# Optimization experiments

Hardware: AMD Instinct MI355X
Metric: run time of the kernel (lower is better)

## Reference

```python
import math
import jax, jax.numpy as jnp
import numpy as np

H = 12  # n_heads
NEG = -1e9

def setup_inputs() -> dict:
    key = jax.random.key(0)
    ks = jax.random.split(key, 5)
    B, S, D = 1, 4096, 768
    x = jax.random.normal(ks[0], (B, S, D), dtype=jnp.float32)
    Wqkv = jax.random.normal(ks[1], (D, 3 * D), dtype=jnp.float32) * (1.0 / math.sqrt(D))
    bqkv = jnp.zeros((3 * D,), dtype=jnp.float32)
    Wout = jax.random.normal(ks[2], (D, D), dtype=jnp.float32) * (1.0 / math.sqrt(D))
    bout = jnp.zeros((D,), dtype=jnp.float32)
    rel_bias = jax.random.normal(ks[3], (H, S, S), dtype=jnp.float32) * 0.02
    # additive causal mask: 0 on/below diagonal, large negative above
    causal_mask = jnp.where(jnp.tril(jnp.ones((S, S), dtype=bool)), 0.0, NEG).astype(jnp.float32)
    return {"x": x, "Wqkv": Wqkv, "bqkv": bqkv, "Wout": Wout, "bout": bout,
            "rel_bias": rel_bias, "causal_mask": causal_mask}

def reference(x, Wqkv, bqkv, Wout, bout, rel_bias, causal_mask):
    B, S, D = x.shape
    hd = D // H
    qkv = x @ Wqkv + bqkv                      # [B,S,3D]
    q, k, v = jnp.split(qkv, 3, axis=-1)
    def heads(t):  # [B,S,D] -> [B,H,S,hd]
        return t.reshape(B, S, H, hd).transpose(0, 2, 1, 3)
    q, k, v = heads(q), heads(k), heads(v)
    scores = jnp.einsum('bhqd,bhkd->bhqk', q, k) / math.sqrt(hd)
    scores = scores + rel_bias[None] + causal_mask[None, None]
    attn = jax.nn.softmax(scores, axis=-1)     # dropout p=0.0 -> identity
    out = jnp.einsum('bhqk,bhkd->bhqd', attn, v)
    out = out.transpose(0, 2, 1, 3).reshape(B, S, D)
    return out @ Wout + bout
```

## Files before the change

### kernel.cpp

```cpp
#include <hip/hip_runtime.h>
#include <stdint.h>

typedef _Float16 f16;
typedef _Float16 f16x8 __attribute__((ext_vector_type(8)));
typedef _Float16 f16x4 __attribute__((ext_vector_type(4)));
typedef float f32x4 __attribute__((ext_vector_type(4)));

#define NEGF -1e30f

static __device__ __forceinline__ f32x4 mfma16(f16x8 a, f16x8 b, f32x4 c) {
    return __builtin_amdgcn_mfma_f32_16x16x32_f16(a, b, c, 0, 0, 0);
}

static __device__ __forceinline__ void gload_lds16(const void* g, void* l) {
    __builtin_amdgcn_global_load_lds(
        (const __attribute__((address_space(1))) unsigned int*)g,
        (__attribute__((address_space(3))) unsigned int*)l, 16, 0, 0);
}

__global__ void cast_f32_f16(const float* __restrict__ src, f16* __restrict__ dst, int n) {
    int idx = blockIdx.x * blockDim.x + threadIdx.x;
    int stride = gridDim.x * blockDim.x;
    for (int i = idx * 4; i < n; i += stride * 4) {
        float4 v = *(const float4*)(src + i);
        f16x4 h;
        h[0] = (f16)v.x; h[1] = (f16)v.y; h[2] = (f16)v.z; h[3] = (f16)v.w;
        *(f16x4*)(dst + i) = h;
    }
}

__global__ void transpose_cast(const float* __restrict__ src, f16* __restrict__ dst, int R, int C) {
    __shared__ float tile[32][33];
    const int c0 = blockIdx.x * 32, r0 = blockIdx.y * 32;
    const int tx = threadIdx.x & 31, ty = threadIdx.x >> 5;
#pragma unroll
    for (int i = 0; i < 32; i += 8)
        tile[ty + i][tx] = src[(size_t)(r0 + ty + i) * C + c0 + tx];
    __syncthreads();
#pragma unroll
    for (int i = 0; i < 32; i += 8)
        dst[(size_t)(c0 + ty + i) * R + r0 + tx] = (f16)tile[tx][ty + i];
}

template <int MODE>
__global__ void __launch_bounds__(256, 2)
gemm_f16(const f16* __restrict__ A, const f16* __restrict__ Bt,
         const float* __restrict__ bias,
         f16* __restrict__ Qb, f16* __restrict__ Kb, f16* __restrict__ Vtb,
         float* __restrict__ Cout, int K, int N) {
    __shared__ alignas(16) f16 As[128 * 32];
    __shared__ alignas(16) f16 Bs[128 * 32];
    const int t = threadIdx.x;
    const int lane = t & 63, wid = t >> 6;
    const int wm = wid >> 1, wn = wid & 1;
    const int lr = lane & 15, lg = lane >> 4;
    const int m0 = blockIdx.y * 128, n0 = blockIdx.x * 128;
    f32x4 acc[4][4] = {};
    for (int k0 = 0; k0 < K; k0 += 32) {
#pragma unroll
        for (int i = 0; i < 2; i++) {
            const int cc = t + i * 256;
            const int rr = cc >> 2, ch = cc & 3;
            gload_lds16(A + (size_t)(m0 + rr) * K + k0 + ch * 8, (f16*)As + cc * 8);
            gload_lds16(Bt + (size_t)(n0 + rr) * K + k0 + ch * 8, (f16*)Bs + cc * 8);
        }
        __syncthreads();
        f16x8 af[4], bf[4];
#pragma unroll
        for (int i = 0; i < 4; i++)
            af[i] = *(const f16x8*)(As + (wm * 64 + i * 16 + lr) * 32 + lg * 8);
#pragma unroll
        for (int j = 0; j < 4; j++)
            bf[j] = *(const f16x8*)(Bs + (wn * 64 + j * 16 + lr) * 32 + lg * 8);
#pragma unroll
        for (int i = 0; i < 4; i++)
#pragma unroll
            for (int j = 0; j < 4; j++)
                acc[i][j] = mfma16(af[i], bf[j], acc[i][j]);
        __syncthreads();
    }
#pragma unroll
    for (int i = 0; i < 4; i++) {
#pragma unroll
        for (int j = 0; j < 4; j++) {
            const int n_g = n0 + wn * 64 + j * 16 + lr;
            const float bv = bias[n_g];
#pragma unroll
            for (int jj = 0; jj < 4; jj++) {
                const int m_g = m0 + wm * 64 + i * 16 + lg * 4 + jj;
                const float val = acc[i][j][jj] + bv;
                if (MODE == 0) {
                    if (n_g < 768) {
                        Qb[(((n_g >> 6) * 4096) + m_g) * 64 + (n_g & 63)] = (f16)(val * 0.125f);
                    } else if (n_g < 1536) {
                        const int n2 = n_g - 768;
                        Kb[(((n2 >> 6) * 4096) + m_g) * 64 + (n2 & 63)] = (f16)val;
                    } else {
                        const int n2 = n_g - 1536;
                        Vtb[((n2 >> 6) * 64 + (n2 & 63)) * 4096 + m_g] = (f16)val;
                    }
                } else {
                    Cout[(size_t)m_g * N + n_g] = val;
                }
            }
        }
    }
}

__global__ void __launch_bounds__(256, 3)
attn_fwd(const f16* __restrict__ Qb, const f16* __restrict__ Kb,
         const f16* __restrict__ Vtb, const float* __restrict__ rel_bias,
         f16* __restrict__ Opart, float* __restrict__ mpart, float* __restrict__ lpart) {
    __shared__ alignas(16) f16 Ks[64 * 64];
    __shared__ alignas(16) f16 Vs[64 * 64];
    __shared__ alignas(16) f16 Ps[4][32 * 72];
    __shared__ alignas(16) float fac[4][32];
    const int bid = blockIdx.x;
    const int h = bid / 144;
    int rr = bid % 144;
    int qb = 0;
    for (;;) { const int n = (qb + 4) >> 2; if (rr < n) break; rr -= n; ++qb; }
    const int c = rr;
    const int lo = c * 8;
    const int hi = min(lo + 8, 2 * qb + 2);

    const int t = threadIdx.x, lane = t & 63, wid = t >> 6;
    const int lr = lane & 15, lg = lane >> 4;
    const int g = qb * 4 + wid;
    const int q0w = g * 32;
    const int ktd = g >> 1;
    const f16* Qh = Qb + (size_t)h * 4096 * 64;
    const f16* Kh = Kb + (size_t)h * 4096 * 64;
    const f16* Vh = Vtb + (size_t)h * 64 * 4096;
    const float* rbh = rel_bias + (size_t)h * 4096 * 4096;

    f16x8 qf[2][2];
#pragma unroll
    for (int nf = 0; nf < 2; nf++)
#pragma unroll
        for (int kd = 0; kd < 2; kd++)
            qf[nf][kd] = *(const f16x8*)(Qh + (size_t)(q0w + nf * 16 + lr) * 64 + kd * 32 + lg * 8);

    f32x4 o[2][4] = {};
    float mrow[2] = {NEGF, NEGF};
    float lrow[2] = {0.f, 0.f};

    for (int kt = lo; kt < hi; kt++) {
        const int kbase = kt * 64;
#pragma unroll
        for (int i = 0; i < 2; i++) {
            const int cc = t + i * 256;
            const int row = cc >> 3;
            const int cswz = (((cc & 7) * 16) ^ ((row & 7) << 4)) >> 1;
            gload_lds16(Kh + (size_t)(kbase + row) * 64 + cswz, (f16*)Ks + cc * 8);
            gload_lds16(Vh + (size_t)row * 4096 + kbase + cswz, (f16*)Vs + cc * 8);
        }
        __syncthreads();
        if (kt <= ktd) {
            float4 rb[2][4];
#pragma unroll
            for (int nf = 0; nf < 2; nf++)
#pragma unroll
                for (int mf = 0; mf < 4; mf++)
                    rb[nf][mf] = *(const float4*)(rbh + (size_t)(q0w + nf * 16 + lr) * 4096 + kbase + mf * 16 + lg * 4);
            f32x4 st[4][2] = {};
#pragma unroll
            for (int kd = 0; kd < 2; kd++) {
#pragma unroll
                for (int mf = 0; mf < 4; mf++) {
                    const int r = mf * 16 + lr;
                    const int cf = ((kd * 64 + lg * 16) ^ ((r & 7) << 4)) >> 1;
                    const f16x8 kf = *(const f16x8*)(Ks + r * 64 + cf);
#pragma unroll
                    for (int nf = 0; nf < 2; nf++)
                        st[mf][nf] = mfma16(kf, qf[nf][kd], st[mf][nf]);
                }
            }
            const bool diag = (kt == ktd);
#pragma unroll
            for (int nf = 0; nf < 2; nf++) {
                const int q_g = q0w + nf * 16 + lr;
                float mx = NEGF;
#pragma unroll
                for (int mf = 0; mf < 4; mf++) {
                    const float rbv[4] = {rb[nf][mf].x, rb[nf][mf].y, rb[nf][mf].z, rb[nf][mf].w};
#pragma unroll
                    for (int jj = 0; jj < 4; jj++) {
                        float v = st[mf][nf][jj] + rbv[jj];
                        if (diag) {
                            const int k_g = kbase + mf * 16 + lg * 4 + jj;
                            v = (k_g > q_g) ? NEGF : v;
                        }
                        st[mf][nf][jj] = v;
                        mx = fmaxf(mx, v);
                    }
                }
                mx = fmaxf(mx, __shfl_xor(mx, 16));
                mx = fmaxf(mx, __shfl_xor(mx, 32));
                const float mnew = fmaxf(mrow[nf], mx);
                const float fscale = __expf(mrow[nf] - mnew);
                mrow[nf] = mnew;
                float rsum = 0.f;
#pragma unroll
                for (int mf = 0; mf < 4; mf++) {
                    f16x4 pv;
#pragma unroll
                    for (int jj = 0; jj < 4; jj++) {
                        const float p = __expf(st[mf][nf][jj] - mnew);
                        rsum += p;
                        pv[jj] = (f16)p;
                    }
                    *(f16x4*)(&Ps[wid][(nf * 16 + lr) * 72 + mf * 16 + lg * 4]) = pv;
                }
                rsum += __shfl_xor(rsum, 16);
                rsum += __shfl_xor(rsum, 32);
                lrow[nf] = lrow[nf] * fscale + rsum;
                if (lane < 16) fac[wid][nf * 16 + lr] = fscale;
            }
            asm volatile("s_waitcnt lgkmcnt(0)" ::: "memory");
#pragma unroll
            for (int qf2 = 0; qf2 < 2; qf2++) {
                const float4 fv = *(const float4*)&fac[wid][qf2 * 16 + lg * 4];
                const float fvv[4] = {fv.x, fv.y, fv.z, fv.w};
#pragma unroll
                for (int df = 0; df < 4; df++)
#pragma unroll
                    for (int jj = 0; jj < 4; jj++)
                        o[qf2][df][jj] *= fvv[jj];
            }
#pragma unroll
            for (int kk = 0; kk < 2; kk++) {
                f16x8 pa[2], vb[4];
#pragma unroll
                for (int qf2 = 0; qf2 < 2; qf2++)
                    pa[qf2] = *(const f16x8*)(&Ps[wid][(qf2 * 16 + lr) * 72 + kk * 32 + lg * 8]);
#pragma unroll
                for (int df = 0; df < 4; df++) {
                    const int r = df * 16 + lr;
                    const int cf = ((kk * 64 + lg * 16) ^ ((r & 7) << 4)) >> 1;
                    vb[df] = *(const f16x8*)(Vs + r * 64 + cf);
                }
#pragma unroll
                for (int qf2 = 0; qf2 < 2; qf2++)
#pragma unroll
                    for (int df = 0; df < 4; df++)
                        o[qf2][df] = mfma16(pa[qf2], vb[df], o[qf2][df]);
            }
        }
        __syncthreads();
    }

    const int s = (h * 128 + g) * 8 + c;
    f16* Op = Opart + (size_t)s * 2048;
#pragma unroll
    for (int qf2 = 0; qf2 < 2; qf2++)
#pragma unroll
        for (int df = 0; df < 4; df++)
#pragma unroll
            for (int jj = 0; jj < 4; jj++)
                Op[(qf2 * 16 + lg * 4 + jj) * 64 + df * 16 + lr] = (f16)o[qf2][df][jj];
    if (lg == 0) {
#pragma unroll
        for (int nf = 0; nf < 2; nf++) {
            mpart[(size_t)s * 32 + nf * 16 + lr] = mrow[nf];
            lpart[(size_t)s * 32 + nf * 16 + lr] = lrow[nf];
        }
    }
}

__global__ void __launch_bounds__(256)
merge_norm(const f16* __restrict__ Opart, const float* __restrict__ mpart,
           const float* __restrict__ lpart, f16* __restrict__ Ob) {
    __shared__ float wls[8][32];
    __shared__ float Linv[32];
    const int g = blockIdx.x, h = blockIdx.y;
    const int nc = (g >> 4) + 1;
    const size_t sb = (size_t)(h * 128 + g) * 8;
    const int t = threadIdx.x;
    if (t < 32) {
        float M = NEGF;
#pragma unroll
        for (int i = 0; i < 8; i++)
            if (i < nc) M = fmaxf(M, mpart[(sb + i) * 32 + t]);
        float L = 0.f;
#pragma unroll
        for (int i = 0; i < 8; i++)
            if (i < nc) {
                const float w = __expf(mpart[(sb + i) * 32 + t] - M);
                wls[i][t] = w;
                L += w * lpart[(sb + i) * 32 + t];
            }
        Linv[t] = 1.f / L;
    }
    __syncthreads();
    const int row = t >> 3, dq = t & 7;
    float acc[8] = {};
#pragma unroll
    for (int i = 0; i < 8; i++) {
        if (i < nc) {
            const f16x8 a = *(const f16x8*)(Opart + (sb + i) * 2048 + row * 64 + dq * 8);
            const float w = wls[i][row];
#pragma unroll
            for (int j = 0; j < 8; j++) acc[j] += w * (float)a[j];
        }
    }
    const float inv = Linv[row];
    const int q = g * 32 + row;
    f16x8 ov;
#pragma unroll
    for (int j = 0; j < 8; j++) ov[j] = (f16)(acc[j] * inv);
    *(f16x8*)(Ob + (size_t)q * 768 + h * 64 + dq * 8) = ov;
}

extern "C" void kernel_launch(void* const* d_in, const int* in_sizes, int n_in,
                              void* d_out, int out_size, void* d_ws, size_t ws_size,
                              hipStream_t stream) {
    const float* x = (const float*)d_in[0];
    const float* Wqkv = (const float*)d_in[1];
    const float* bqkv = (const float*)d_in[2];
    const float* Wout = (const float*)d_in[3];
    const float* bout = (const float*)d_in[4];
    const float* rel_bias = (const float*)d_in[5];
    float* out = (float*)d_out;

    f16* p = (f16*)d_ws;
    f16* xb = p;     p += (size_t)4096 * 768;
    f16* WqkvT = p;  p += (size_t)2304 * 768;
    f16* WoutT = p;  p += (size_t)768 * 768;
    f16* Qb = p;     p += (size_t)12 * 4096 * 64;
    f16* Kb = p;     p += (size_t)12 * 4096 * 64;
    f16* Vtb = p;    p += (size_t)12 * 4096 * 64;
    f16* Ob = p;     p += (size_t)4096 * 768;
    f16* Opart = p;  p += (size_t)12 * 128 * 8 * 2048;
    float* fp = (float*)p;
    float* mpart = fp;  fp += (size_t)12 * 128 * 8 * 32;
    float* lpart = fp;  fp += (size_t)12 * 128 * 8 * 32;

    cast_f32_f16<<<3072, 256, 0, stream>>>(x, xb, 4096 * 768);
    transpose_cast<<<dim3(2304 / 32, 768 / 32), 256, 0, stream>>>(Wqkv, WqkvT, 768, 2304);
    transpose_cast<<<dim3(768 / 32, 768 / 32), 256, 0, stream>>>(Wout, WoutT, 768, 768);
    gemm_f16<0><<<dim3(18, 32), 256, 0, stream>>>(xb, WqkvT, bqkv, Qb, Kb, Vtb, nullptr, 768, 2304);
    attn_fwd<<<dim3(1728), 256, 0, stream>>>(Qb, Kb, Vtb, rel_bias, Opart, mpart, lpart);
    merge_norm<<<dim3(128, 12), 256, 0, stream>>>(Opart, mpart, lpart, Ob);
    gemm_f16<1><<<dim3(6, 32), 256, 0, stream>>>(Ob, WoutT, bout, nullptr, nullptr, nullptr, out, 768, 768);
}
```

Before: 225.1 us.

## Double-buffer LDS tiles in GEMMs and attention, retile output projection

```diff
diff --git a/kernel.cpp b/kernel.cpp
--- a/kernel.cpp
+++ b/kernel.cpp
@@ -42,36 +42,42 @@
         dst[(size_t)(c0 + ty + i) * R + r0 + tx] = (f16)tile[tx][ty + i];
 }
 
-template <int MODE>
 __global__ void __launch_bounds__(256, 2)
-gemm_f16(const f16* __restrict__ A, const f16* __restrict__ Bt,
+gemm_qkv(const f16* __restrict__ A, const f16* __restrict__ Bt,
          const float* __restrict__ bias,
-         f16* __restrict__ Qb, f16* __restrict__ Kb, f16* __restrict__ Vtb,
-         float* __restrict__ Cout, int K, int N) {
-    __shared__ alignas(16) f16 As[128 * 32];
-    __shared__ alignas(16) f16 Bs[128 * 32];
+         f16* __restrict__ Qb, f16* __restrict__ Kb, f16* __restrict__ Vtb, int K) {
+    __shared__ alignas(16) f16 As[2][128 * 32];
+    __shared__ alignas(16) f16 Bs[2][128 * 32];
     const int t = threadIdx.x;
     const int lane = t & 63, wid = t >> 6;
     const int wm = wid >> 1, wn = wid & 1;
     const int lr = lane & 15, lg = lane >> 4;
     const int m0 = blockIdx.y * 128, n0 = blockIdx.x * 128;
-    f32x4 acc[4][4] = {};
-    for (int k0 = 0; k0 < K; k0 += 32) {
+
+    auto stage = [&](int buf, int k0) {
 #pragma unroll
         for (int i = 0; i < 2; i++) {
             const int cc = t + i * 256;
             const int rr = cc >> 2, ch = cc & 3;
-            gload_lds16(A + (size_t)(m0 + rr) * K + k0 + ch * 8, (f16*)As + cc * 8);
-            gload_lds16(Bt + (size_t)(n0 + rr) * K + k0 + ch * 8, (f16*)Bs + cc * 8);
-        }
-        __syncthreads();
+            gload_lds16(A + (size_t)(m0 + rr) * K + k0 + ch * 8, (f16*)As[buf] + cc * 8);
+            gload_lds16(Bt + (size_t)(n0 + rr) * K + k0 + ch * 8, (f16*)Bs[buf] + cc * 8);
+        }
+    };
+
+    f32x4 acc[4][4] = {};
+    stage(0, 0);
+    __syncthreads();
+    const int NK = K / 32;
+    for (int it = 0; it < NK; ++it) {
+        const int cur = it & 1;
+        if (it + 1 < NK) stage(cur ^ 1, (it + 1) * 32);
         f16x8 af[4], bf[4];
 #pragma unroll
         for (int i = 0; i < 4; i++)
-            af[i] = *(const f16x8*)(As + (wm * 64 + i * 16 + lr) * 32 + lg * 8);
+            af[i] = *(const f16x8*)((f16*)As[cur] + (wm * 64 + i * 16 + lr) * 32 + lg * 8);
 #pragma unroll
         for (int j = 0; j < 4; j++)
-            bf[j] = *(const f16x8*)(Bs + (wn * 64 + j * 16 + lr) * 32 + lg * 8);
+            bf[j] = *(const f16x8*)((f16*)Bs[cur] + (wn * 64 + j * 16 + lr) * 32 + lg * 8);
 #pragma unroll
         for (int i = 0; i < 4; i++)
 #pragma unroll
@@ -89,19 +95,72 @@
             for (int jj = 0; jj < 4; jj++) {
                 const int m_g = m0 + wm * 64 + i * 16 + lg * 4 + jj;
                 const float val = acc[i][j][jj] + bv;
-                if (MODE == 0) {
-                    if (n_g < 768) {
-                        Qb[(((n_g >> 6) * 4096) + m_g) * 64 + (n_g & 63)] = (f16)(val * 0.125f);
-                    } else if (n_g < 1536) {
-                        const int n2 = n_g - 768;
-                        Kb[(((n2 >> 6) * 4096) + m_g) * 64 + (n2 & 63)] = (f16)val;
-                    } else {
-                        const int n2 = n_g - 1536;
-                        Vtb[((n2 >> 6) * 64 + (n2 & 63)) * 4096 + m_g] = (f16)val;
-                    }
+                if (n_g < 768) {
+                    Qb[(((n_g >> 6) * 4096) + m_g) * 64 + (n_g & 63)] = (f16)(val * 0.125f);
+                } else if (n_g < 1536) {
+                    const int n2 = n_g - 768;
+                    Kb[(((n2 >> 6) * 4096) + m_g) * 64 + (n2 & 63)] = (f16)val;
                 } else {
-                    Cout[(size_t)m_g * N + n_g] = val;
+                    const int n2 = n_g - 1536;
+                    Vtb[((n2 >> 6) * 64 + (n2 & 63)) * 4096 + m_g] = (f16)val;
                 }
+            }
+        }
+    }
+}
+
+__global__ void __launch_bounds__(256, 3)
+gemm_out(const f16* __restrict__ A, const f16* __restrict__ Bt,
+         const float* __restrict__ bias, float* __restrict__ Cout, int K, int N) {
+    __shared__ alignas(16) f16 As[2][128 * 32];
+    __shared__ alignas(16) f16 Bs[2][64 * 32];
+    const int t = threadIdx.x;
+    const int lane = t & 63, wid = t >> 6;
+    const int lr = lane & 15, lg = lane >> 4;
+    const int m0 = blockIdx.y * 128, n0 = blockIdx.x * 64;
+
+    auto stage = [&](int buf, int k0) {
+#pragma unroll
+        for (int i = 0; i < 2; i++) {
+            const int cc = t + i * 256;
+            const int rr = cc >> 2, ch = cc & 3;
+            gload_lds16(A + (size_t)(m0 + rr) * K + k0 + ch * 8, (f16*)As[buf] + cc * 8);
+        }
+        const int rr = t >> 2, ch = t & 3;
+        gload_lds16(Bt + (size_t)(n0 + rr) * K + k0 + ch * 8, (f16*)Bs[buf] + t * 8);
+    };
+
+    f32x4 acc[2][4] = {};
+    stage(0, 0);
+    __syncthreads();
+    const int NK = K / 32;
+    for (int it = 0; it < NK; ++it) {
+        const int cur = it & 1;
+        if (it + 1 < NK) stage(cur ^ 1, (it + 1) * 32);
+        f16x8 af[2], bf[4];
+#pragma unroll
+        for (int i = 0; i < 2; i++)
+            af[i] = *(const f16x8*)((f16*)As[cur] + (wid * 32 + i * 16 + lr) * 32 + lg * 8);
+#pragma unroll
+        for (int j = 0; j < 4; j++)
+            bf[j] = *(const f16x8*)((f16*)Bs[cur] + (j * 16 + lr) * 32 + lg * 8);
+#pragma unroll
+        for (int i = 0; i < 2; i++)
+#pragma unroll
+            for (int j = 0; j < 4; j++)
+                acc[i][j] = mfma16(af[i], bf[j], acc[i][j]);
+        __syncthreads();
+    }
+#pragma unroll
+    for (int i = 0; i < 2; i++) {
+#pragma unroll
+        for (int j = 0; j < 4; j++) {
+            const int n_g = n0 + j * 16 + lr;
+            const float bv = bias[n_g];
+#pragma unroll
+            for (int jj = 0; jj < 4; jj++) {
+                const int m_g = m0 + wid * 32 + i * 16 + lg * 4 + jj;
+                Cout[(size_t)m_g * N + n_g] = acc[i][j][jj] + bv;
             }
         }
     }
@@ -111,8 +170,8 @@
 attn_fwd(const f16* __restrict__ Qb, const f16* __restrict__ Kb,
          const f16* __restrict__ Vtb, const float* __restrict__ rel_bias,
          f16* __restrict__ Opart, float* __restrict__ mpart, float* __restrict__ lpart) {
-    __shared__ alignas(16) f16 Ks[64 * 64];
-    __shared__ alignas(16) f16 Vs[64 * 64];
+    __shared__ alignas(16) f16 Ks[2][64 * 64];
+    __shared__ alignas(16) f16 Vs[2][64 * 64];
     __shared__ alignas(16) f16 Ps[4][32 * 72];
     __shared__ alignas(16) float fac[4][32];
     const int bid = blockIdx.x;
@@ -134,28 +193,35 @@
     const f16* Vh = Vtb + (size_t)h * 64 * 4096;
     const float* rbh = rel_bias + (size_t)h * 4096 * 4096;
 
-    f16x8 qf[2][2];
-#pragma unroll
-    for (int nf = 0; nf < 2; nf++)
-#pragma unroll
-        for (int kd = 0; kd < 2; kd++)
-            qf[nf][kd] = *(const f16x8*)(Qh + (size_t)(q0w + nf * 16 + lr) * 64 + kd * 32 + lg * 8);
-
-    f32x4 o[2][4] = {};
-    float mrow[2] = {NEGF, NEGF};
-    float lrow[2] = {0.f, 0.f};
-
-    for (int kt = lo; kt < hi; kt++) {
+    auto stage = [&](int buf, int kt) {
         const int kbase = kt * 64;
 #pragma unroll
         for (int i = 0; i < 2; i++) {
             const int cc = t + i * 256;
             const int row = cc >> 3;
             const int cswz = (((cc & 7) * 16) ^ ((row & 7) << 4)) >> 1;
-            gload_lds16(Kh + (size_t)(kbase + row) * 64 + cswz, (f16*)Ks + cc * 8);
-            gload_lds16(Vh + (size_t)row * 4096 + kbase + cswz, (f16*)Vs + cc * 8);
-        }
-        __syncthreads();
+            gload_lds16(Kh + (size_t)(kbase + row) * 64 + cswz, (f16*)Ks[buf] + cc * 8);
+            gload_lds16(Vh + (size_t)row * 4096 + kbase + cswz, (f16*)Vs[buf] + cc * 8);
+        }
+    };
+
+    f16x8 qf[2][2];
+#pragma unroll
+    for (int nf = 0; nf < 2; nf++)
+#pragma unroll
+        for (int kd = 0; kd < 2; kd++)
+            qf[nf][kd] = *(const f16x8*)(Qh + (size_t)(q0w + nf * 16 + lr) * 64 + kd * 32 + lg * 8);
+
+    f32x4 o[2][4] = {};
+    float mrow[2] = {NEGF, NEGF};
+    float lrow[2] = {0.f, 0.f};
+
+    stage(0, lo);
+    __syncthreads();
+    for (int kt = lo; kt < hi; kt++) {
+        const int kbase = kt * 64;
+        const int cur = (kt - lo) & 1;
+        if (kt + 1 < hi) stage(cur ^ 1, kt + 1);
         if (kt <= ktd) {
             float4 rb[2][4];
 #pragma unroll
@@ -170,7 +236,7 @@
                 for (int mf = 0; mf < 4; mf++) {
                     const int r = mf * 16 + lr;
                     const int cf = ((kd * 64 + lg * 16) ^ ((r & 7) << 4)) >> 1;
-                    const f16x8 kf = *(const f16x8*)(Ks + r * 64 + cf);
+                    const f16x8 kf = *(const f16x8*)((f16*)Ks[cur] + r * 64 + cf);
 #pragma unroll
                     for (int nf = 0; nf < 2; nf++)
                         st[mf][nf] = mfma16(kf, qf[nf][kd], st[mf][nf]);
@@ -238,7 +304,7 @@
                 for (int df = 0; df < 4; df++) {
                     const int r = df * 16 + lr;
                     const int cf = ((kk * 64 + lg * 16) ^ ((r & 7) << 4)) >> 1;
-                    vb[df] = *(const f16x8*)(Vs + r * 64 + cf);
+                    vb[df] = *(const f16x8*)((f16*)Vs[cur] + r * 64 + cf);
                 }
 #pragma unroll
                 for (int qf2 = 0; qf2 < 2; qf2++)
@@ -339,8 +405,8 @@
     cast_f32_f16<<<3072, 256, 0, stream>>>(x, xb, 4096 * 768);
     transpose_cast<<<dim3(2304 / 32, 768 / 32), 256, 0, stream>>>(Wqkv, WqkvT, 768, 2304);
     transpose_cast<<<dim3(768 / 32, 768 / 32), 256, 0, stream>>>(Wout, WoutT, 768, 768);
-    gemm_f16<0><<<dim3(18, 32), 256, 0, stream>>>(xb, WqkvT, bqkv, Qb, Kb, Vtb, nullptr, 768, 2304);
+    gemm_qkv<<<dim3(18, 32), 256, 0, stream>>>(xb, WqkvT, bqkv, Qb, Kb, Vtb, 768);
     attn_fwd<<<dim3(1728), 256, 0, stream>>>(Qb, Kb, Vtb, rel_bias, Opart, mpart, lpart);
     merge_norm<<<dim3(128, 12), 256, 0, stream>>>(Opart, mpart, lpart, Ob);
-    gemm_f16<1><<<dim3(6, 32), 256, 0, stream>>>(Ob, WoutT, bout, nullptr, nullptr, nullptr, out, 768, 768);
-}
+    gemm_out<<<dim3(12, 32), 256, 0, stream>>>(Ob, WoutT, bout, out, 768, 768);
+}
```

New measurement: 199.4 us. 1.13x faster.
